# Performance work log

Hardware: AMD Instinct MI355X
Metric: run time of the kernel (lower is better)

Reference implementation:

```python
import jax, jax.numpy as jnp
import numpy as np


def setup_inputs() -> dict:
    key = jax.random.key(0)
    k1, k2 = jax.random.split(key)
    N, H, W = 8, 64, 128
    flow = jax.random.normal(k1, (N, 2, H, W), dtype=jnp.float32)
    mask = jax.random.normal(k2, (N, 9 * 8 * 8, H, W), dtype=jnp.float32)
    return {"flow": flow, "mask": mask}


def reference(flow, mask):
    # flow: [N, 2, H, W], mask: [N, 576, H, W] -> up_flow: [N, 2, 8H, 8W]
    N, C, H, W = flow.shape  # C == 2
    m = mask.reshape(N, 9, 8, 8, H, W)  # (torch view had a leading 1-dim; broadcast instead)
    m = jax.nn.softmax(m, axis=1)  # softmax over the 9 neighbor weights

    # F.unfold(8*flow, [3,3], padding=1): 3x3 neighborhoods, row-major kernel order
    f = 8.0 * flow
    fp = jnp.pad(f, ((0, 0), (0, 0), (1, 1), (1, 1)))
    # patches: [N, 2, 9, H, W], k = di*3 + dj matches unfold's ordering per channel
    patches = jnp.stack(
        [fp[:, :, di:di + H, dj:dj + W] for di in range(3) for dj in range(3)],
        axis=2,
    )

    # convex combination: sum over the 9 neighbors -> [N, 2, 8, 8, H, W]
    up = jnp.einsum("nkabhw,nckhw->ncabhw", m, patches)
    # permute (0,1,4,2,5,3): [N, 2, H, 8, W, 8] then merge -> [N, 2, 8H, 8W]
    up = jnp.transpose(up, (0, 1, 4, 2, 5, 3))
    return up.reshape(N, C, 8 * H, 8 * W)
```

## Files before the change

### kernel.cpp

```cpp
#include <hip/hip_runtime.h>


#define N_ 8
#define H_ 64
#define W_ 128
#define HW_ (H_ * W_)

__global__ __launch_bounds__(128, 4) void flow_up_kernel(
    const float* __restrict__ flow,
    const float* __restrict__ mask,
    float* __restrict__ out)
{
    const int bid = blockIdx.x;
    const int a = bid & 7;
    const int h = (bid >> 3) & (H_ - 1);
    const int n = bid >> 9;
    const int w = threadIdx.x;

    float p0[9], p1[9];
    const float* __restrict__ f0 = flow + (n * 2 + 0) * HW_;
    const float* __restrict__ f1 = flow + (n * 2 + 1) * HW_;
#pragma unroll
    for (int di = 0; di < 3; ++di) {
        const int hr = h - 1 + di;
        const int hc = min(max(hr, 0), H_ - 1);
        const bool hin = (hr >= 0) && (hr < H_);
#pragma unroll
        for (int dj = 0; dj < 3; ++dj) {
            const int wr = w - 1 + dj;
            const int wc = min(max(wr, 0), W_ - 1);
            const float sc = (hin && wr >= 0 && wr < W_) ? 8.0f : 0.0f;
            const int o = hc * W_ + wc;
            p0[di * 3 + dj] = f0[o] * sc;
            p1[di * 3 + dj] = f1[o] * sc;
        }
    }

    const float* __restrict__ mp = mask + (n * 576 + a * 8) * HW_ + h * W_ + w;

    float acc0[8], acc1[8];
#pragma unroll
    for (int b = 0; b < 8; ++b) {
        float s = 0.0f, o0 = 0.0f, o1 = 0.0f;
#pragma unroll
        for (int k = 0; k < 9; ++k) {
            const float e = __expf(mp[(k * 64 + b) * HW_]);
            s  += e;
            o0 += e * p0[k];
            o1 += e * p1[k];
        }
        const float inv = __builtin_amdgcn_rcpf(s);
        acc0[b] = o0 * inv;
        acc1[b] = o1 * inv;
    }

    const int y = h * 8 + a;
    float4* __restrict__ q0 = (float4*)(out + ((n * 2 + 0) * (8 * H_) + y) * (8 * W_) + 8 * w);
    float4* __restrict__ q1 = (float4*)(out + ((n * 2 + 1) * (8 * H_) + y) * (8 * W_) + 8 * w);
    q0[0] = make_float4(acc0[0], acc0[1], acc0[2], acc0[3]);
    q0[1] = make_float4(acc0[4], acc0[5], acc0[6], acc0[7]);
    q1[0] = make_float4(acc1[0], acc1[1], acc1[2], acc1[3]);
    q1[1] = make_float4(acc1[4], acc1[5], acc1[6], acc1[7]);
}

extern "C" void kernel_launch(void* const* d_in, const int* in_sizes, int n_in,
                              void* d_out, int out_size, void* d_ws, size_t ws_size,
                              hipStream_t stream) {
    const float* flow = (const float*)d_in[0];
    const float* mask = (const float*)d_in[1];
    float* out = (float*)d_out;

    const int grid = N_ * H_ * 8;
    flow_up_kernel<<<grid, 128, 0, stream>>>(flow, mask, out);
}
```

Measured before the change: 224.5 us.

## Remap threads to subpixel-by-4-pixel work with float4 mask loads

Each thread now owns one subpixel column b and four adjacent source pixels, instead of one pixel and all eight subpixels. It issues nine float4 mask loads rather than 72 scalar loads, and keeps a 3x6 flow window in registers that the four pixels share. The block grows to 256 threads so the 8 subpixels times 128 width are still covered. The cost is that output stores become scalar and strided (8-float runs every 32 floats) instead of contiguous float4 writes, which may hurt write coalescing.

```diff
diff --git a/kernel.cpp b/kernel.cpp
--- a/kernel.cpp
+++ b/kernel.cpp
@@ -6,7 +6,7 @@
 #define W_ 128
 #define HW_ (H_ * W_)
 
-__global__ __launch_bounds__(128, 4) void flow_up_kernel(
+__global__ __launch_bounds__(256, 4) void flow_up_kernel(
     const float* __restrict__ flow,
     const float* __restrict__ mask,
     float* __restrict__ out)
@@ -15,9 +15,11 @@
     const int a = bid & 7;
     const int h = (bid >> 3) & (H_ - 1);
     const int n = bid >> 9;
-    const int w = threadIdx.x;
+    const int t = threadIdx.x;
+    const int b = t & 7;
+    const int w4 = (t >> 3) << 2;
 
-    float p0[9], p1[9];
+    float r0[3][6], r1[3][6];
     const float* __restrict__ f0 = flow + (n * 2 + 0) * HW_;
     const float* __restrict__ f1 = flow + (n * 2 + 1) * HW_;
 #pragma unroll
@@ -26,41 +28,42 @@
         const int hc = min(max(hr, 0), H_ - 1);
         const bool hin = (hr >= 0) && (hr < H_);
 #pragma unroll
-        for (int dj = 0; dj < 3; ++dj) {
-            const int wr = w - 1 + dj;
+        for (int j = 0; j < 6; ++j) {
+            const int wr = w4 - 1 + j;
             const int wc = min(max(wr, 0), W_ - 1);
             const float sc = (hin && wr >= 0 && wr < W_) ? 8.0f : 0.0f;
-            const int o = hc * W_ + wc;
-            p0[di * 3 + dj] = f0[o] * sc;
-            p1[di * 3 + dj] = f1[o] * sc;
+            r0[di][j] = f0[hc * W_ + wc] * sc;
+            r1[di][j] = f1[hc * W_ + wc] * sc;
         }
     }
 
-    const float* __restrict__ mp = mask + (n * 576 + a * 8) * HW_ + h * W_ + w;
+    const float4* __restrict__ mp =
+        (const float4*)(mask + (n * 576 + a * 8 + b) * HW_ + h * W_ + w4);
 
-    float acc0[8], acc1[8];
+    float ss[4] = {0.f, 0.f, 0.f, 0.f};
+    float o0[4] = {0.f, 0.f, 0.f, 0.f};
+    float o1[4] = {0.f, 0.f, 0.f, 0.f};
 #pragma unroll
-    for (int b = 0; b < 8; ++b) {
-        float s = 0.0f, o0 = 0.0f, o1 = 0.0f;
-#pragma unroll
-        for (int k = 0; k < 9; ++k) {
-            const float e = __expf(mp[(k * 64 + b) * HW_]);
-            s  += e;
-            o0 += e * p0[k];
-            o1 += e * p1[k];
-        }
-        const float inv = __builtin_amdgcn_rcpf(s);
-        acc0[b] = o0 * inv;
-        acc1[b] = o1 * inv;
+    for (int k = 0; k < 9; ++k) {
+        const int di = k / 3, dj = k % 3;
+        const float4 m = mp[k * 16 * HW_];
+        const float e0 = __expf(m.x), e1 = __expf(m.y),
+                    e2 = __expf(m.z), e3 = __expf(m.w);
+        ss[0] += e0; o0[0] += e0 * r0[di][dj + 0]; o1[0] += e0 * r1[di][dj + 0];
+        ss[1] += e1; o0[1] += e1 * r0[di][dj + 1]; o1[1] += e1 * r1[di][dj + 1];
+        ss[2] += e2; o0[2] += e2 * r0[di][dj + 2]; o1[2] += e2 * r1[di][dj + 2];
+        ss[3] += e3; o0[3] += e3 * r0[di][dj + 3]; o1[3] += e3 * r1[di][dj + 3];
     }
 
     const int y = h * 8 + a;
-    float4* __restrict__ q0 = (float4*)(out + ((n * 2 + 0) * (8 * H_) + y) * (8 * W_) + 8 * w);
-    float4* __restrict__ q1 = (float4*)(out + ((n * 2 + 1) * (8 * H_) + y) * (8 * W_) + 8 * w);
-    q0[0] = make_float4(acc0[0], acc0[1], acc0[2], acc0[3]);
-    q0[1] = make_float4(acc0[4], acc0[5], acc0[6], acc0[7]);
-    q1[0] = make_float4(acc1[0], acc1[1], acc1[2], acc1[3]);
-    q1[1] = make_float4(acc1[4], acc1[5], acc1[6], acc1[7]);
+    float* __restrict__ q0 = out + ((n * 2 + 0) * (8 * H_) + y) * (8 * W_) + 8 * w4 + b;
+    float* __restrict__ q1 = out + ((n * 2 + 1) * (8 * H_) + y) * (8 * W_) + 8 * w4 + b;
+#pragma unroll
+    for (int wi = 0; wi < 4; ++wi) {
+        const float inv = __builtin_amdgcn_rcpf(ss[wi]);
+        q0[8 * wi] = o0[wi] * inv;
+        q1[8 * wi] = o1[wi] * inv;
+    }
 }
 
 extern "C" void kernel_launch(void* const* d_in, const int* in_sizes, int n_in,
@@ -71,5 +74,5 @@
     float* out = (float*)d_out;
 
     const int grid = N_ * H_ * 8;
-    flow_up_kernel<<<grid, 128, 0, stream>>>(flow, mask, out);
+    flow_up_kernel<<<grid, 256, 0, stream>>>(flow, mask, out);
 }
```

Measured after the change: 220.9 us (median of 2 runs). No clear change (-1.6%).
